# Kernel tuning notes

Hardware: AMD Instinct MI355X
Metric: run time of the kernel (lower is better)

The kernel has to match this reference:

```python
import jax, jax.numpy as jnp
import numpy as np

B, H, N, D, RPE = 2, 8, 4096, 64, 64
LAYERS = 3


def _rms(x):
    # SimpleRMSNorm: x / sqrt(mean(x^2) + eps), no learned scale
    return x / jnp.sqrt(jnp.mean(x * x, axis=-1, keepdims=True) + 1e-8)


def setup_inputs() -> dict:
    key = jax.random.key(0)
    ks = jax.random.split(key, 7)
    s = 1.0 / np.sqrt(RPE)
    return {
        "x": jax.random.normal(ks[0], (B, H, N, D), dtype=jnp.float32),
        "w_in": jax.random.normal(ks[1], (1, RPE), dtype=jnp.float32) * 0.5,
        "b_in": jax.random.normal(ks[2], (RPE,), dtype=jnp.float32) * 0.02,
        "w_hid": jax.random.normal(ks[3], (LAYERS, RPE, RPE), dtype=jnp.float32) * s,
        "b_hid": jax.random.normal(ks[4], (LAYERS, RPE), dtype=jnp.float32) * 0.02,
        "w_out": jax.random.normal(ks[5], (RPE, H * D), dtype=jnp.float32) * s,
        "b_out": jax.random.normal(ks[6], (H * D,), dtype=jnp.float32) * 0.02,
    }


def reference(x, w_in, b_in, w_hid, b_hid, w_out, b_out):
    n = x.shape[-2]
    dt = x.dtype

    def rpe(idx):  # idx: (m, 1) relative-position features
        h = idx @ w_in + b_in  # (m, RPE)
        for i in range(LAYERS):  # non-residual: x = layer(x)
            h = jax.nn.relu(_rms(h)) @ w_hid[i] + b_hid[i]
        h = jax.nn.relu(_rms(h)) @ w_out + b_out  # (m, H*D)
        return h.reshape(-1, H, D).transpose(1, 0, 2)  # (H, m, D)

    zero_idx = jnp.ones((1, 1), dt)
    pos_idx = (1.0 / jnp.arange(2, n + 1, dtype=dt)).reshape(n - 1, 1)
    neg_idx = (-1.0 / jnp.arange(n, 1, -1, dtype=dt)).reshape(n - 1, 1)

    zero_k = rpe(zero_idx)  # (H, 1, D); used for both T[0] slots like the torch code
    a = jnp.concatenate([zero_k, rpe(pos_idx), zero_k, rpe(neg_idx)], axis=1)  # (H, 2n, D)
    # act_type='none' -> identity activation on a

    # Toeplitz matvec as circular conv of length 2n via FFT
    y = jnp.fft.rfft(x, 2 * n, axis=-2)          # (B, H, n+1, D) complex
    v = jnp.fft.rfft(a, 2 * n, axis=-2)[None]    # (1, H, n+1, D) complex
    out = jnp.fft.irfft(v * y, 2 * n, axis=-2)[:, :, :n, :]
    return out.astype(dt)
```

## Files before the change

kernel.cpp:

```cpp
#include <hip/hip_runtime.h>

#define N_SEQ 4096
#define N_FFT 8192
#define LAYERS 3
#define FT 512
#define PIDX(i) ((i) + ((i) >> 5))

template<int M>
__device__ inline void pass16_fwd(float* re, float* im, int tid)
{
    const int Q = M >> 4;
    const int j = tid & (Q - 1);
    const int G = tid / Q;
    const int base = G * M + j;
    const float KR[4] = {1.f, 0.9238795325f, 0.7071067812f, 0.3826834324f};
    const float KI[4] = {0.f, -0.3826834324f, -0.7071067812f, -0.9238795325f};
    float xr[4][4], xi[4][4];
#pragma unroll
    for (int a = 0; a < 4; ++a)
#pragma unroll
        for (int b = 0; b < 4; ++b) {
            int idx = PIDX(base + a * (M >> 2) + b * Q);
            xr[a][b] = re[idx]; xi[a][b] = im[idx];
        }
    float cj, sj;
    __sincosf(-6.283185307179586f / (float)M * (float)j, &sj, &cj);
#pragma unroll
    for (int b = 0; b < 4; ++b) {
        float c1 = cj * KR[b] - sj * KI[b];
        float s1 = cj * KI[b] + sj * KR[b];
        float c2 = c1 * c1 - s1 * s1, s2 = 2.f * c1 * s1;
        float c3 = c2 * c1 - s2 * s1, s3 = c2 * s1 + s2 * c1;
        float ar = xr[0][b] + xr[2][b], ai = xi[0][b] + xi[2][b];
        float br = xr[0][b] - xr[2][b], bi = xi[0][b] - xi[2][b];
        float cr = xr[1][b] + xr[3][b], ci = xi[1][b] + xi[3][b];
        float dr = xi[1][b] - xi[3][b], di = -(xr[1][b] - xr[3][b]);
        xr[0][b] = ar + cr;               xi[0][b] = ai + ci;
        float t1r = br + dr, t1i = bi + di;
        xr[1][b] = t1r * c1 - t1i * s1;   xi[1][b] = t1r * s1 + t1i * c1;
        float t2r = ar - cr, t2i = ai - ci;
        xr[2][b] = t2r * c2 - t2i * s2;   xi[2][b] = t2r * s2 + t2i * c2;
        float t3r = br - dr, t3i = bi - di;
        xr[3][b] = t3r * c3 - t3i * s3;   xi[3][b] = t3r * s3 + t3i * c3;
    }
    {
        float e1c = cj * cj - sj * sj, e1s = 2.f * cj * sj;
        float c1 = e1c * e1c - e1s * e1s, s1 = 2.f * e1c * e1s;
        float c2 = c1 * c1 - s1 * s1, s2 = 2.f * c1 * s1;
        float c3 = c2 * c1 - s2 * s1, s3 = c2 * s1 + s2 * c1;
#pragma unroll
        for (int a = 0; a < 4; ++a) {
            float ar = xr[a][0] + xr[a][2], ai = xi[a][0] + xi[a][2];
            float br = xr[a][0] - xr[a][2], bi = xi[a][0] - xi[a][2];
            float cr = xr[a][1] + xr[a][3], ci = xi[a][1] + xi[a][3];
            float dr = xi[a][1] - xi[a][3], di = -(xr[a][1] - xr[a][3]);
            xr[a][0] = ar + cr;               xi[a][0] = ai + ci;
            float t1r = br + dr, t1i = bi + di;
            xr[a][1] = t1r * c1 - t1i * s1;   xi[a][1] = t1r * s1 + t1i * c1;
            float t2r = ar - cr, t2i = ai - ci;
            xr[a][2] = t2r * c2 - t2i * s2;   xi[a][2] = t2r * s2 + t2i * c2;
            float t3r = br - dr, t3i = bi - di;
            xr[a][3] = t3r * c3 - t3i * s3;   xi[a][3] = t3r * s3 + t3i * c3;
        }
    }
#pragma unroll
    for (int a = 0; a < 4; ++a)
#pragma unroll
        for (int b = 0; b < 4; ++b) {
            int idx = PIDX(base + a * (M >> 2) + b * Q);
            re[idx] = xr[a][b]; im[idx] = xi[a][b];
        }
}

template<int M>
__device__ inline void pass16_inv(float* re, float* im, int tid)
{
    const int Q = M >> 4;
    const int j = tid & (Q - 1);
    const int G = tid / Q;
    const int base = G * M + j;
    const float KR[4] = {1.f, 0.9238795325f, 0.7071067812f, 0.3826834324f};
    const float KI[4] = {0.f, 0.3826834324f, 0.7071067812f, 0.9238795325f};
    float xr[4][4], xi[4][4];
#pragma unroll
    for (int a = 0; a < 4; ++a)
#pragma unroll
        for (int b = 0; b < 4; ++b) {
            int idx = PIDX(base + a * (M >> 2) + b * Q);
            xr[a][b] = re[idx]; xi[a][b] = im[idx];
        }
    float cj, sj;
    __sincosf(6.283185307179586f / (float)M * (float)j, &sj, &cj);
    {
        float e1c = cj * cj - sj * sj, e1s = 2.f * cj * sj;
        float c1 = e1c * e1c - e1s * e1s, s1 = 2.f * e1c * e1s;
        float c2 = c1 * c1 - s1 * s1, s2 = 2.f * c1 * s1;
        float c3 = c2 * c1 - s2 * s1, s3 = c2 * s1 + s2 * c1;
#pragma unroll
        for (int a = 0; a < 4; ++a) {
            float t0r = xr[a][0], t0i = xi[a][0];
            float t1r = xr[a][1] * c1 - xi[a][1] * s1, t1i = xr[a][1] * s1 + xi[a][1] * c1;
            float t2r = xr[a][2] * c2 - xi[a][2] * s2, t2i = xr[a][2] * s2 + xi[a][2] * c2;
            float t3r = xr[a][3] * c3 - xi[a][3] * s3, t3i = xr[a][3] * s3 + xi[a][3] * c3;
            float pr = t0r + t2r, pi = t0i + t2i;
            float qr = t0r - t2r, qi = t0i - t2i;
            float rr = t1r + t3r, ri = t1i + t3i;
            float sr = -(t1i - t3i), si = t1r - t3r;
            xr[a][0] = pr + rr; xi[a][0] = pi + ri;
            xr[a][1] = qr + sr; xi[a][1] = qi + si;
            xr[a][2] = pr - rr; xi[a][2] = pi - ri;
            xr[a][3] = qr - sr; xi[a][3] = qi - si;
        }
    }
#pragma unroll
    for (int b = 0; b < 4; ++b) {
        float c1 = cj * KR[b] - sj * KI[b];
        float s1 = cj * KI[b] + sj * KR[b];
        float c2 = c1 * c1 - s1 * s1, s2 = 2.f * c1 * s1;
        float c3 = c2 * c1 - s2 * s1, s3 = c2 * s1 + s2 * c1;
        float t0r = xr[0][b], t0i = xi[0][b];
        float t1r = xr[1][b] * c1 - xi[1][b] * s1, t1i = xr[1][b] * s1 + xi[1][b] * c1;
        float t2r = xr[2][b] * c2 - xi[2][b] * s2, t2i = xr[2][b] * s2 + xi[2][b] * c2;
        float t3r = xr[3][b] * c3 - xi[3][b] * s3, t3i = xr[3][b] * s3 + xi[3][b] * c3;
        float pr = t0r + t2r, pi = t0i + t2i;
        float qr = t0r - t2r, qi = t0i - t2i;
        float rr = t1r + t3r, ri = t1i + t3i;
        float sr = -(t1i - t3i), si = t1r - t3r;
        xr[0][b] = pr + rr; xi[0][b] = pi + ri;
        xr[1][b] = qr + sr; xi[1][b] = qi + si;
        xr[2][b] = pr - rr; xi[2][b] = pi - ri;
        xr[3][b] = qr - sr; xi[3][b] = qi - si;
    }
#pragma unroll
    for (int a = 0; a < 4; ++a)
#pragma unroll
        for (int b = 0; b < 4; ++b) {
            int idx = PIDX(base + a * (M >> 2) + b * Q);
            re[idx] = xr[a][b]; im[idx] = xi[a][b];
        }
}

__device__ inline void fwd8(float* zr, float* zi, int o)
{
    const float R = 0.70710678118654752f;
    {
        float ar = zr[o] + zr[o+4], ai = zi[o] + zi[o+4];
        float br = zr[o] - zr[o+4], bi = zi[o] - zi[o+4];
        float cr = zr[o+2] + zr[o+6], ci = zi[o+2] + zi[o+6];
        float dr = zi[o+2] - zi[o+6], di = -(zr[o+2] - zr[o+6]);
        zr[o]   = ar + cr; zi[o]   = ai + ci;
        zr[o+2] = br + dr; zi[o+2] = bi + di;
        zr[o+4] = ar - cr; zi[o+4] = ai - ci;
        zr[o+6] = br - dr; zi[o+6] = bi - di;
    }
    {
        float ar = zr[o+1] + zr[o+5], ai = zi[o+1] + zi[o+5];
        float br = zr[o+1] - zr[o+5], bi = zi[o+1] - zi[o+5];
        float cr = zr[o+3] + zr[o+7], ci = zi[o+3] + zi[o+7];
        float dr = zi[o+3] - zi[o+7], di = -(zr[o+3] - zr[o+7]);
        zr[o+1] = ar + cr; zi[o+1] = ai + ci;
        float t1r = br + dr, t1i = bi + di;
        zr[o+3] = R * (t1r + t1i); zi[o+3] = R * (t1i - t1r);
        float t2r = ar - cr, t2i = ai - ci;
        zr[o+5] = t2i;  zi[o+5] = -t2r;
        float t3r = br - dr, t3i = bi - di;
        zr[o+7] = R * (t3i - t3r); zi[o+7] = -R * (t3r + t3i);
    }
#pragma unroll
    for (int p = 0; p < 8; p += 2) {
        float ur = zr[o+p], ui = zi[o+p], vr = zr[o+p+1], vi = zi[o+p+1];
        zr[o+p]   = ur + vr; zi[o+p]   = ui + vi;
        zr[o+p+1] = ur - vr; zi[o+p+1] = ui - vi;
    }
}

__device__ inline void inv8(float* zr, float* zi, int o)
{
    const float R = 0.70710678118654752f;
#pragma unroll
    for (int p = 0; p < 8; p += 2) {
        float ur = zr[o+p], ui = zi[o+p], vr = zr[o+p+1], vi = zi[o+p+1];
        zr[o+p]   = ur + vr; zi[o+p]   = ui + vi;
        zr[o+p+1] = ur - vr; zi[o+p+1] = ui - vi;
    }
    {
        float t0r = zr[o],   t0i = zi[o];
        float t1r = zr[o+2], t1i = zi[o+2];
        float t2r = zr[o+4], t2i = zi[o+4];
        float t3r = zr[o+6], t3i = zi[o+6];
        float pr = t0r + t2r, pi = t0i + t2i;
        float qr = t0r - t2r, qi = t0i - t2i;
        float rr = t1r + t3r, ri = t1i + t3i;
        float sr = -(t1i - t3i), si = t1r - t3r;
        zr[o]   = pr + rr; zi[o]   = pi + ri;
        zr[o+2] = qr + sr; zi[o+2] = qi + si;
        zr[o+4] = pr - rr; zi[o+4] = pi - ri;
        zr[o+6] = qr - sr; zi[o+6] = qi - si;
    }
    {
        float t0r = zr[o+1], t0i = zi[o+1];
        float yr = zr[o+3], yi = zi[o+3];
        float t1r = R * (yr - yi), t1i = R * (yr + yi);
        yr = zr[o+5]; yi = zi[o+5];
        float t2r = -yi, t2i = yr;
        yr = zr[o+7]; yi = zi[o+7];
        float t3r = -R * (yr + yi), t3i = R * (yr - yi);
        float pr = t0r + t2r, pi = t0i + t2i;
        float qr = t0r - t2r, qi = t0i - t2i;
        float rr = t1r + t3r, ri = t1i + t3i;
        float sr = -(t1i - t3i), si = t1r - t3r;
        zr[o+1] = pr + rr; zi[o+1] = pi + ri;
        zr[o+3] = qr + sr; zi[o+3] = qi + si;
        zr[o+5] = pr - rr; zi[o+5] = pi - ri;
        zr[o+7] = qr - sr; zi[o+7] = qi - si;
    }
}

__global__ __launch_bounds__(512, 4) void prep_kernel(
    const float* __restrict__ x,
    const float* __restrict__ w_in, const float* __restrict__ b_in,
    const float* __restrict__ w_hid, const float* __restrict__ b_hid,
    const float* __restrict__ w_out, const float* __restrict__ b_out,
    float* __restrict__ a_t, float2* __restrict__ xt2)
{
    __shared__ __align__(16) char smem[33536];
    const int tid = threadIdx.x;

    if (blockIdx.x >= 128) {
        float (*t0)[65] = (float (*)[65])smem;
        float (*t1)[65] = (float (*)[65])(smem + 16640);
        int bb = blockIdx.x - 128;
        int h = bb >> 6;
        int nb = bb & 63;
        int lx = tid & 63;
        int ly = tid >> 6;
        const float* s0 = x + ((size_t)h * N_SEQ + nb * 64) * 64;
        const float* s1 = x + ((size_t)(8 + h) * N_SEQ + nb * 64) * 64;
        for (int r = ly; r < 64; r += 8) {
            t0[r][lx] = s0[r * 64 + lx];
            t1[r][lx] = s1[r * 64 + lx];
        }
        __syncthreads();
        for (int r = ly; r < 64; r += 8) {
            float2* dst = xt2 + (size_t)(h * 64 + r) * N_SEQ + nb * 64;
            dst[lx] = make_float2(t0[lx][r], t1[lx][r]);
        }
        return;
    }

    float (*ubuf)[65] = (float (*)[65])smem;
    float (*sums)[9]  = (float (*)[9])(smem + 16640);
    const int p = tid & 63;
    const int w = __builtin_amdgcn_readfirstlane(tid >> 6);
    const int pos = blockIdx.x * 64 + p;

    float v;
    if (pos == 0 || pos == N_SEQ) v = 1.0f;
    else if (pos < N_SEQ)         v = 1.0f / (float)(pos + 1);
    else                          v = -1.0f / (float)(2 * N_SEQ + 1 - pos);

    float h[8];
#pragma unroll
    for (int i = 0; i < 8; ++i) {
        int f = w * 8 + i;
        h[i] = v * w_in[f] + b_in[f];
    }
    for (int L = 0; L < LAYERS; ++L) {
        float s = 0.f;
#pragma unroll
        for (int i = 0; i < 8; ++i) s += h[i] * h[i];
        sums[p][w] = s;
        __syncthreads();
        float tot = 0.f;
#pragma unroll
        for (int g = 0; g < 8; ++g) tot += sums[p][g];
        float r = rsqrtf(tot * (1.f / 64.f) + 1e-8f);
#pragma unroll
        for (int i = 0; i < 8; ++i)
            ubuf[p][w * 8 + i] = fmaxf(h[i] * r, 0.f);
        __syncthreads();
        float acc[8];
        const float* bh = b_hid + L * 64 + w * 8;
#pragma unroll
        for (int i = 0; i < 8; ++i) acc[i] = bh[i];
        const float* wbase = w_hid + L * 4096 + w * 8;
        for (int j = 0; j < 64; ++j) {
            float uj = ubuf[p][j];
            const float* wr = wbase + j * 64;
#pragma unroll
            for (int i = 0; i < 8; ++i)
                acc[i] = fmaf(uj, wr[i], acc[i]);
        }
#pragma unroll
        for (int i = 0; i < 8; ++i) h[i] = acc[i];
    }
    {
        float s = 0.f;
#pragma unroll
        for (int i = 0; i < 8; ++i) s += h[i] * h[i];
        sums[p][w] = s;
        __syncthreads();
        float tot = 0.f;
#pragma unroll
        for (int g = 0; g < 8; ++g) tot += sums[p][g];
        float r = rsqrtf(tot * (1.f / 64.f) + 1e-8f);
#pragma unroll
        for (int i = 0; i < 8; ++i)
            ubuf[p][w * 8 + i] = fmaxf(h[i] * r, 0.f);
        __syncthreads();
    }
    {
        const int c = w;
        float acc[64];
        const float* bo = b_out + c * 64;
#pragma unroll
        for (int f = 0; f < 64; ++f) acc[f] = bo[f];
        const float* wbase = w_out + c * 64;
        for (int j = 0; j < 64; ++j) {
            float uj = ubuf[p][j];
            const float* wr = wbase + j * 512;
#pragma unroll
            for (int f = 0; f < 64; ++f)
                acc[f] = fmaf(uj, wr[f], acc[f]);
        }
        float* dst = a_t + pos;
#pragma unroll
        for (int f = 0; f < 64; ++f)
            dst[(size_t)(c * 64 + f) * N_FFT] = acc[f];
    }
}

__global__ __launch_bounds__(FT, 2) void conv_kernel(const float* __restrict__ a_t,
                                                     const float2* __restrict__ xt2,
                                                     float2* __restrict__ out_t2)
{
    __shared__ float re[8448];
    __shared__ float im[8448];
    const int tid = threadIdx.x;
    const int hd = blockIdx.x;
    const float JR = 0.9238795325f;
    const float JI = -0.3826834324f;

    {
        const float* src = a_t + (size_t)hd * N_FFT;
        float ck, sk;
        __sincosf(-6.283185307179586f / 8192.f * (float)tid, &sk, &ck);
#pragma unroll
        for (int pp = 0; pp < 4; ++pp) {
            int k = pp * FT + tid;
            float x0 = src[k], x1 = src[k + 2048], x2 = src[k + 4096], x3 = src[k + 6144];
            float ar = x0 + x2, br = x0 - x2;
            float cr = x1 + x3, e = x1 - x3;
            re[PIDX(k)] = ar + cr; im[PIDX(k)] = 0.f;
            float c1 = ck, s1 = sk;
            float c2 = c1 * c1 - s1 * s1, s2 = 2.f * c1 * s1;
            float c3 = c2 * c1 - s2 * s1, s3 = c2 * s1 + s2 * c1;
            re[PIDX(k + 2048)] = br * c1 + e * s1;  im[PIDX(k + 2048)] = br * s1 - e * c1;
            float t2r = ar - cr;
            re[PIDX(k + 4096)] = t2r * c2;          im[PIDX(k + 4096)] = t2r * s2;
            re[PIDX(k + 6144)] = br * c3 - e * s3;  im[PIDX(k + 6144)] = br * s3 + e * c3;
            float tc = ck * JR - sk * JI; sk = ck * JI + sk * JR; ck = tc;
        }
    }
    __syncthreads();
    pass16_fwd<2048>(re, im, tid);
    __syncthreads();
    pass16_fwd<128>(re, im, tid);
    __syncthreads();
    float afr[16], afi[16];
    {
        const int base = tid * 16;
#pragma unroll
        for (int c = 0; c < 16; ++c) { int idx = PIDX(base + c); afr[c] = re[idx]; afi[c] = im[idx]; }
        fwd8(afr, afi, 0); fwd8(afr, afi, 8);
    }
    __syncthreads();
    {
        const float2* src = xt2 + (size_t)hd * N_SEQ;
        float ck, sk;
        __sincosf(-6.283185307179586f / 8192.f * (float)tid, &sk, &ck);
#pragma unroll
        for (int pp = 0; pp < 4; ++pp) {
            int k = pp * FT + tid;
            float2 z0 = src[k], z1 = src[k + 2048];
            float ar = z0.x, ai = z0.y;
            float cr = z1.x, ci = z1.y;
            float dr = z1.y, di = -z1.x;
            re[PIDX(k)] = ar + cr; im[PIDX(k)] = ai + ci;
            float c1 = ck, s1 = sk;
            float c2 = c1 * c1 - s1 * s1, s2 = 2.f * c1 * s1;
            float c3 = c2 * c1 - s2 * s1, s3 = c2 * s1 + s2 * c1;
            float t1r = ar + dr, t1i = ai + di;
            re[PIDX(k + 2048)] = t1r * c1 - t1i * s1; im[PIDX(k + 2048)] = t1r * s1 + t1i * c1;
            float t2r = ar - cr, t2i = ai - ci;
            re[PIDX(k + 4096)] = t2r * c2 - t2i * s2; im[PIDX(k + 4096)] = t2r * s2 + t2i * c2;
            float t3r = ar - dr, t3i = ai - di;
            re[PIDX(k + 6144)] = t3r * c3 - t3i * s3; im[PIDX(k + 6144)] = t3r * s3 + t3i * c3;
            float tc = ck * JR - sk * JI; sk = ck * JI + sk * JR; ck = tc;
        }
    }
    __syncthreads();
    pass16_fwd<2048>(re, im, tid);
    __syncthreads();
    pass16_fwd<128>(re, im, tid);
    __syncthreads();
    {
        const int base = tid * 16;
        float zr[16], zi[16];
#pragma unroll
        for (int c = 0; c < 16; ++c) { int idx = PIDX(base + c); zr[c] = re[idx]; zi[c] = im[idx]; }
        fwd8(zr, zi, 0); fwd8(zr, zi, 8);
        const float inv = 1.0f / (float)N_FFT;
#pragma unroll
        for (int c = 0; c < 16; ++c) {
            float xr = zr[c], xi_ = zi[c];
            zr[c] = (xr * afr[c] - xi_ * afi[c]) * inv;
            zi[c] = (xr * afi[c] + xi_ * afr[c]) * inv;
        }
        inv8(zr, zi, 0); inv8(zr, zi, 8);
#pragma unroll
        for (int c = 0; c < 16; ++c) { int idx = PIDX(base + c); re[idx] = zr[c]; im[idx] = zi[c]; }
    }
    __syncthreads();
    pass16_inv<128>(re, im, tid);
    __syncthreads();
    pass16_inv<2048>(re, im, tid);
    __syncthreads();
    {
        float2* dst = out_t2 + (size_t)hd * N_SEQ;
        float ck, sk;
        __sincosf(6.283185307179586f / 8192.f * (float)tid, &sk, &ck);
        const float JcR = 0.9238795325f, JcI = 0.3826834324f;
#pragma unroll
        for (int pp = 0; pp < 4; ++pp) {
            int k = pp * FT + tid;
            float c1 = ck, s1 = sk;
            float c2 = c1 * c1 - s1 * s1, s2 = 2.f * c1 * s1;
            float c3 = c2 * c1 - s2 * s1, s3 = c2 * s1 + s2 * c1;
            float t0r = re[PIDX(k)],        t0i = im[PIDX(k)];
            float y1r = re[PIDX(k + 2048)], y1i = im[PIDX(k + 2048)];
            float y2r = re[PIDX(k + 4096)], y2i = im[PIDX(k + 4096)];
            float y3r = re[PIDX(k + 6144)], y3i = im[PIDX(k + 6144)];
            float t1r = y1r * c1 - y1i * s1, t1i = y1r * s1 + y1i * c1;
            float t2r = y2r * c2 - y2i * s2, t2i = y2r * s2 + y2i * c2;
            float t3r = y3r * c3 - y3i * s3, t3i = y3r * s3 + y3i * c3;
            float pr = t0r + t2r, pi = t0i + t2i;
            float qr = t0r - t2r, qi = t0i - t2i;
            float rr = t1r + t3r, ri = t1i + t3i;
            float sr = -(t1i - t3i), si = t1r - t3r;
            dst[k]        = make_float2(pr + rr, pi + ri);
            dst[k + 2048] = make_float2(qr + sr, qi + si);
            float tc = ck * JcR - sk * JcI; sk = ck * JcI + sk * JcR; ck = tc;
        }
    }
}

__global__ __launch_bounds__(256) void transpose_o_kernel(const float2* __restrict__ out_t2,
                                                          float* __restrict__ out)
{
    __shared__ float t0[64][65];
    __shared__ float t1[64][65];
    int h = blockIdx.x >> 6;
    int nb = blockIdx.x & 63;
    int lx = threadIdx.x & 63;
    int ly = threadIdx.x >> 6;
    for (int r = ly; r < 64; r += 4) {
        float2 v = out_t2[(size_t)(h * 64 + r) * N_SEQ + nb * 64 + lx];
        t0[r][lx] = v.x;
        t1[r][lx] = v.y;
    }
    __syncthreads();
    float* d0 = out + ((size_t)h * N_SEQ + nb * 64) * 64;
    float* d1 = out + ((size_t)(8 + h) * N_SEQ + nb * 64) * 64;
    for (int r = ly; r < 64; r += 4) {
        d0[r * 64 + lx] = t0[lx][r];
        d1[r * 64 + lx] = t1[lx][r];
    }
}

extern "C" void kernel_launch(void* const* d_in, const int* in_sizes, int n_in,
                              void* d_out, int out_size, void* d_ws, size_t ws_size,
                              hipStream_t stream)
{
    const float* x     = (const float*)d_in[0];
    const float* w_in  = (const float*)d_in[1];
    const float* b_in  = (const float*)d_in[2];
    const float* w_hid = (const float*)d_in[3];
    const float* b_hid = (const float*)d_in[4];
    const float* w_out = (const float*)d_in[5];
    const float* b_out = (const float*)d_in[6];
    float* out = (float*)d_out;

    char* ws = (char*)d_ws;
    float2* xt2    = (float2*)ws;
    float*  a_t    = (float*)(ws + (size_t)16 * 1024 * 1024);
    float2* out_t2 = (float2*)(ws + (size_t)32 * 1024 * 1024);

    prep_kernel<<<640, 512, 0, stream>>>(x, w_in, b_in, w_hid, b_hid, w_out, b_out,
                                         a_t, xt2);
    conv_kernel<<<512, FT, 0, stream>>>(a_t, xt2, out_t2);
    transpose_o_kernel<<<512, 256, 0, stream>>>(out_t2, out);
}
```

Measured before the change: 160.6 us.

## Register-tile prep MLP matmuls and halve prep block size

Result: slower. 164.2 us (+2.2%).

```diff
diff --git a/kernel.cpp b/kernel.cpp
--- a/kernel.cpp
+++ b/kernel.cpp
@@ -216,7 +216,7 @@
     }
 }
 
-__global__ __launch_bounds__(512, 4) void prep_kernel(
+__global__ __launch_bounds__(256, 2) void prep_kernel(
     const float* __restrict__ x,
     const float* __restrict__ w_in, const float* __restrict__ b_in,
     const float* __restrict__ w_hid, const float* __restrict__ b_hid,
@@ -236,97 +236,134 @@
         int ly = tid >> 6;
         const float* s0 = x + ((size_t)h * N_SEQ + nb * 64) * 64;
         const float* s1 = x + ((size_t)(8 + h) * N_SEQ + nb * 64) * 64;
-        for (int r = ly; r < 64; r += 8) {
+        for (int r = ly; r < 64; r += 4) {
             t0[r][lx] = s0[r * 64 + lx];
             t1[r][lx] = s1[r * 64 + lx];
         }
         __syncthreads();
-        for (int r = ly; r < 64; r += 8) {
+        for (int r = ly; r < 64; r += 4) {
             float2* dst = xt2 + (size_t)(h * 64 + r) * N_SEQ + nb * 64;
             dst[lx] = make_float2(t0[lx][r], t1[lx][r]);
         }
         return;
     }
 
-    float (*ubuf)[65] = (float (*)[65])smem;
-    float (*sums)[9]  = (float (*)[9])(smem + 16640);
-    const int p = tid & 63;
-    const int w = __builtin_amdgcn_readfirstlane(tid >> 6);
-    const int pos = blockIdx.x * 64 + p;
-
-    float v;
-    if (pos == 0 || pos == N_SEQ) v = 1.0f;
-    else if (pos < N_SEQ)         v = 1.0f / (float)(pos + 1);
-    else                          v = -1.0f / (float)(2 * N_SEQ + 1 - pos);
-
-    float h[8];
-#pragma unroll
-    for (int i = 0; i < 8; ++i) {
-        int f = w * 8 + i;
-        h[i] = v * w_in[f] + b_in[f];
-    }
-    for (int L = 0; L < LAYERS; ++L) {
-        float s = 0.f;
-#pragma unroll
-        for (int i = 0; i < 8; ++i) s += h[i] * h[i];
-        sums[p][w] = s;
-        __syncthreads();
-        float tot = 0.f;
-#pragma unroll
-        for (int g = 0; g < 8; ++g) tot += sums[p][g];
-        float r = rsqrtf(tot * (1.f / 64.f) + 1e-8f);
-#pragma unroll
-        for (int i = 0; i < 8; ++i)
-            ubuf[p][w * 8 + i] = fmaxf(h[i] * r, 0.f);
-        __syncthreads();
-        float acc[8];
-        const float* bh = b_hid + L * 64 + w * 8;
-#pragma unroll
-        for (int i = 0; i < 8; ++i) acc[i] = bh[i];
-        const float* wbase = w_hid + L * 4096 + w * 8;
-        for (int j = 0; j < 64; ++j) {
-            float uj = ubuf[p][j];
-            const float* wr = wbase + j * 64;
-#pragma unroll
-            for (int i = 0; i < 8; ++i)
-                acc[i] = fmaf(uj, wr[i], acc[i]);
-        }
-#pragma unroll
-        for (int i = 0; i < 8; ++i) h[i] = acc[i];
-    }
-    {
-        float s = 0.f;
-#pragma unroll
-        for (int i = 0; i < 8; ++i) s += h[i] * h[i];
-        sums[p][w] = s;
-        __syncthreads();
-        float tot = 0.f;
-#pragma unroll
-        for (int g = 0; g < 8; ++g) tot += sums[p][g];
-        float r = rsqrtf(tot * (1.f / 64.f) + 1e-8f);
-#pragma unroll
-        for (int i = 0; i < 8; ++i)
-            ubuf[p][w * 8 + i] = fmaxf(h[i] * r, 0.f);
-        __syncthreads();
-    }
-    {
-        const int c = w;
-        float acc[64];
-        const float* bo = b_out + c * 64;
-#pragma unroll
-        for (int f = 0; f < 64; ++f) acc[f] = bo[f];
-        const float* wbase = w_out + c * 64;
-        for (int j = 0; j < 64; ++j) {
-            float uj = ubuf[p][j];
-            const float* wr = wbase + j * 512;
-#pragma unroll
-            for (int f = 0; f < 64; ++f)
-                acc[f] = fmaf(uj, wr[f], acc[f]);
-        }
-        float* dst = a_t + pos;
-#pragma unroll
-        for (int f = 0; f < 64; ++f)
-            dst[(size_t)(c * 64 + f) * N_FFT] = acc[f];
+    float (*ubuf)[68] = (float (*)[68])smem;
+    float (*sums)[68] = (float (*)[68])(smem + 17408);
+    const int pos0 = blockIdx.x * 64;
+
+    {
+        const int pq = tid & 15;
+        const int fq = tid >> 4;
+        float v[4];
+#pragma unroll
+        for (int k = 0; k < 4; ++k) {
+            int pos = pos0 + pq * 4 + k;
+            if (pos == 0 || pos == N_SEQ) v[k] = 1.0f;
+            else if (pos < N_SEQ)         v[k] = 1.0f / (float)(pos + 1);
+            else                          v[k] = -1.0f / (float)(2 * N_SEQ + 1 - pos);
+        }
+        float h[4][4];
+#pragma unroll
+        for (int i = 0; i < 4; ++i) {
+            float wi = w_in[fq * 4 + i], bi = b_in[fq * 4 + i];
+#pragma unroll
+            for (int k = 0; k < 4; ++k) h[i][k] = v[k] * wi + bi;
+        }
+        for (int L = 0; L <= LAYERS; ++L) {
+            float4 ss = make_float4(0.f, 0.f, 0.f, 0.f);
+#pragma unroll
+            for (int i = 0; i < 4; ++i) {
+                ss.x += h[i][0] * h[i][0]; ss.y += h[i][1] * h[i][1];
+                ss.z += h[i][2] * h[i][2]; ss.w += h[i][3] * h[i][3];
+            }
+            *(float4*)&sums[fq][pq * 4] = ss;
+            __syncthreads();
+            float4 tot = make_float4(0.f, 0.f, 0.f, 0.f);
+#pragma unroll
+            for (int g = 0; g < 16; ++g) {
+                float4 s4 = *(const float4*)&sums[g][pq * 4];
+                tot.x += s4.x; tot.y += s4.y; tot.z += s4.z; tot.w += s4.w;
+            }
+            float r[4] = {rsqrtf(tot.x * (1.f/64.f) + 1e-8f),
+                          rsqrtf(tot.y * (1.f/64.f) + 1e-8f),
+                          rsqrtf(tot.z * (1.f/64.f) + 1e-8f),
+                          rsqrtf(tot.w * (1.f/64.f) + 1e-8f)};
+#pragma unroll
+            for (int i = 0; i < 4; ++i) {
+                float4 u4;
+                u4.x = fmaxf(h[i][0] * r[0], 0.f);
+                u4.y = fmaxf(h[i][1] * r[1], 0.f);
+                u4.z = fmaxf(h[i][2] * r[2], 0.f);
+                u4.w = fmaxf(h[i][3] * r[3], 0.f);
+                *(float4*)&ubuf[fq * 4 + i][pq * 4] = u4;
+            }
+            __syncthreads();
+            if (L == LAYERS) break;
+            float acc[4][4];
+#pragma unroll
+            for (int i = 0; i < 4; ++i) {
+                float bi = b_hid[L * 64 + fq * 4 + i];
+#pragma unroll
+                for (int k = 0; k < 4; ++k) acc[i][k] = bi;
+            }
+            const float* wb = w_hid + L * 4096 + fq * 4;
+#pragma unroll 4
+            for (int j = 0; j < 64; ++j) {
+                float4 u4 = *(const float4*)&ubuf[j][pq * 4];
+                float4 w4 = *(const float4*)(wb + j * 64);
+                acc[0][0] = fmaf(u4.x, w4.x, acc[0][0]); acc[0][1] = fmaf(u4.y, w4.x, acc[0][1]);
+                acc[0][2] = fmaf(u4.z, w4.x, acc[0][2]); acc[0][3] = fmaf(u4.w, w4.x, acc[0][3]);
+                acc[1][0] = fmaf(u4.x, w4.y, acc[1][0]); acc[1][1] = fmaf(u4.y, w4.y, acc[1][1]);
+                acc[1][2] = fmaf(u4.z, w4.y, acc[1][2]); acc[1][3] = fmaf(u4.w, w4.y, acc[1][3]);
+                acc[2][0] = fmaf(u4.x, w4.z, acc[2][0]); acc[2][1] = fmaf(u4.y, w4.z, acc[2][1]);
+                acc[2][2] = fmaf(u4.z, w4.z, acc[2][2]); acc[2][3] = fmaf(u4.w, w4.z, acc[2][3]);
+                acc[3][0] = fmaf(u4.x, w4.w, acc[3][0]); acc[3][1] = fmaf(u4.y, w4.w, acc[3][1]);
+                acc[3][2] = fmaf(u4.z, w4.w, acc[3][2]); acc[3][3] = fmaf(u4.w, w4.w, acc[3][3]);
+            }
+#pragma unroll
+            for (int i = 0; i < 4; ++i)
+#pragma unroll
+                for (int k = 0; k < 4; ++k) h[i][k] = acc[i][k];
+        }
+    }
+
+    {
+        const int wv = tid >> 6;
+        const int lane = tid & 63;
+        const int po = lane & 7;
+        const int fo = lane >> 3;
+        for (int rnd = 0; rnd < 2; ++rnd) {
+            const int c = rnd * 4 + wv;
+            float acc[8][8];
+#pragma unroll
+            for (int i = 0; i < 8; ++i) {
+                float bo = b_out[c * 64 + fo * 8 + i];
+#pragma unroll
+                for (int k = 0; k < 8; ++k) acc[i][k] = bo;
+            }
+            const float* wb = w_out + c * 64 + fo * 8;
+#pragma unroll 2
+            for (int j = 0; j < 64; ++j) {
+                float4 u0 = *(const float4*)&ubuf[j][po * 8];
+                float4 u1 = *(const float4*)&ubuf[j][po * 8 + 4];
+                float4 w0 = *(const float4*)(wb + j * 512);
+                float4 w1 = *(const float4*)(wb + j * 512 + 4);
+                float wv_[8] = {w0.x, w0.y, w0.z, w0.w, w1.x, w1.y, w1.z, w1.w};
+                float uv_[8] = {u0.x, u0.y, u0.z, u0.w, u1.x, u1.y, u1.z, u1.w};
+#pragma unroll
+                for (int i = 0; i < 8; ++i)
+#pragma unroll
+                    for (int k = 0; k < 8; ++k)
+                        acc[i][k] = fmaf(uv_[k], wv_[i], acc[i][k]);
+            }
+#pragma unroll
+            for (int i = 0; i < 8; ++i) {
+                float* dst = a_t + (size_t)(c * 64 + fo * 8 + i) * N_FFT + pos0 + po * 8;
+                *(float4*)dst       = make_float4(acc[i][0], acc[i][1], acc[i][2], acc[i][3]);
+                *(float4*)(dst + 4) = make_float4(acc[i][4], acc[i][5], acc[i][6], acc[i][7]);
+            }
+        }
     }
 }
 
@@ -496,7 +533,7 @@
     float*  a_t    = (float*)(ws + (size_t)16 * 1024 * 1024);
     float2* out_t2 = (float2*)(ws + (size_t)32 * 1024 * 1024);
 
-    prep_kernel<<<640, 512, 0, stream>>>(x, w_in, b_in, w_hid, b_hid, w_out, b_out,
+    prep_kernel<<<640, 256, 0, stream>>>(x, w_in, b_in, w_hid, b_hid, w_out, b_out,
                                          a_t, xt2);
     conv_kernel<<<512, FT, 0, stream>>>(a_t, xt2, out_t2);
     transpose_o_kernel<<<512, 256, 0, stream>>>(out_t2, out);
```

## Retile RPE MLP prep kernel with register-blocked output GEMM and vector stores

Applied to the files above, without the earlier changes.

New measurement: 159.5 us. About the same (-0.7%).

```diff
diff --git a/kernel.cpp b/kernel.cpp
--- a/kernel.cpp
+++ b/kernel.cpp
@@ -216,7 +216,7 @@
     }
 }
 
-__global__ __launch_bounds__(512, 4) void prep_kernel(
+__global__ __launch_bounds__(256, 2) void prep_kernel(
     const float* __restrict__ x,
     const float* __restrict__ w_in, const float* __restrict__ b_in,
     const float* __restrict__ w_hid, const float* __restrict__ b_hid,
@@ -226,107 +226,112 @@
     __shared__ __align__(16) char smem[33536];
     const int tid = threadIdx.x;
 
-    if (blockIdx.x >= 128) {
+    if (blockIdx.x >= 256) {
         float (*t0)[65] = (float (*)[65])smem;
         float (*t1)[65] = (float (*)[65])(smem + 16640);
-        int bb = blockIdx.x - 128;
+        int bb = blockIdx.x - 256;
         int h = bb >> 6;
         int nb = bb & 63;
         int lx = tid & 63;
         int ly = tid >> 6;
         const float* s0 = x + ((size_t)h * N_SEQ + nb * 64) * 64;
         const float* s1 = x + ((size_t)(8 + h) * N_SEQ + nb * 64) * 64;
-        for (int r = ly; r < 64; r += 8) {
+        for (int r = ly; r < 64; r += 4) {
             t0[r][lx] = s0[r * 64 + lx];
             t1[r][lx] = s1[r * 64 + lx];
         }
         __syncthreads();
-        for (int r = ly; r < 64; r += 8) {
+        for (int r = ly; r < 64; r += 4) {
             float2* dst = xt2 + (size_t)(h * 64 + r) * N_SEQ + nb * 64;
             dst[lx] = make_float2(t0[lx][r], t1[lx][r]);
         }
         return;
     }
 
-    float (*ubuf)[65] = (float (*)[65])smem;
-    float (*sums)[9]  = (float (*)[9])(smem + 16640);
-    const int p = tid & 63;
-    const int w = __builtin_amdgcn_readfirstlane(tid >> 6);
-    const int pos = blockIdx.x * 64 + p;
-
-    float v;
-    if (pos == 0 || pos == N_SEQ) v = 1.0f;
-    else if (pos < N_SEQ)         v = 1.0f / (float)(pos + 1);
-    else                          v = -1.0f / (float)(2 * N_SEQ + 1 - pos);
-
-    float h[8];
-#pragma unroll
-    for (int i = 0; i < 8; ++i) {
-        int f = w * 8 + i;
-        h[i] = v * w_in[f] + b_in[f];
-    }
-    for (int L = 0; L < LAYERS; ++L) {
-        float s = 0.f;
-#pragma unroll
-        for (int i = 0; i < 8; ++i) s += h[i] * h[i];
-        sums[p][w] = s;
-        __syncthreads();
-        float tot = 0.f;
-#pragma unroll
-        for (int g = 0; g < 8; ++g) tot += sums[p][g];
-        float r = rsqrtf(tot * (1.f / 64.f) + 1e-8f);
-#pragma unroll
-        for (int i = 0; i < 8; ++i)
-            ubuf[p][w * 8 + i] = fmaxf(h[i] * r, 0.f);
-        __syncthreads();
-        float acc[8];
-        const float* bh = b_hid + L * 64 + w * 8;
-#pragma unroll
-        for (int i = 0; i < 8; ++i) acc[i] = bh[i];
-        const float* wbase = w_hid + L * 4096 + w * 8;
-        for (int j = 0; j < 64; ++j) {
-            float uj = ubuf[p][j];
-            const float* wr = wbase + j * 64;
+    float (*ubuf)[36] = (float (*)[36])smem;
+    float (*sums)[9]  = (float (*)[9])(smem + 9216);
+    const int pos0 = blockIdx.x * 32;
+
+    {
+        const int p  = tid & 31;
+        const int fp = tid >> 5;
+        const int pos = pos0 + p;
+        float v;
+        if (pos == 0 || pos == N_SEQ) v = 1.0f;
+        else if (pos < N_SEQ)         v = 1.0f / (float)(pos + 1);
+        else                          v = -1.0f / (float)(2 * N_SEQ + 1 - pos);
+
+        float h[8];
+#pragma unroll
+        for (int i = 0; i < 8; ++i) {
+            int f = fp * 8 + i;
+            h[i] = v * w_in[f] + b_in[f];
+        }
+        for (int L = 0; L <= LAYERS; ++L) {
+            float s = 0.f;
+#pragma unroll
+            for (int i = 0; i < 8; ++i) s += h[i] * h[i];
+            sums[p][fp] = s;
+            __syncthreads();
+            float tot = 0.f;
+#pragma unroll
+            for (int g = 0; g < 8; ++g) tot += sums[p][g];
+            float r = rsqrtf(tot * (1.f / 64.f) + 1e-8f);
 #pragma unroll
             for (int i = 0; i < 8; ++i)
-                acc[i] = fmaf(uj, wr[i], acc[i]);
-        }
-#pragma unroll
-        for (int i = 0; i < 8; ++i) h[i] = acc[i];
-    }
-    {
-        float s = 0.f;
-#pragma unroll
-        for (int i = 0; i < 8; ++i) s += h[i] * h[i];
-        sums[p][w] = s;
-        __syncthreads();
-        float tot = 0.f;
-#pragma unroll
-        for (int g = 0; g < 8; ++g) tot += sums[p][g];
-        float r = rsqrtf(tot * (1.f / 64.f) + 1e-8f);
-#pragma unroll
-        for (int i = 0; i < 8; ++i)
-            ubuf[p][w * 8 + i] = fmaxf(h[i] * r, 0.f);
-        __syncthreads();
-    }
-    {
-        const int c = w;
-        float acc[64];
-        const float* bo = b_out + c * 64;
-#pragma unroll
-        for (int f = 0; f < 64; ++f) acc[f] = bo[f];
-        const float* wbase = w_out + c * 64;
-        for (int j = 0; j < 64; ++j) {
-            float uj = ubuf[p][j];
-            const float* wr = wbase + j * 512;
-#pragma unroll
-            for (int f = 0; f < 64; ++f)
-                acc[f] = fmaf(uj, wr[f], acc[f]);
-        }
-        float* dst = a_t + pos;
-#pragma unroll
-        for (int f = 0; f < 64; ++f)
-            dst[(size_t)(c * 64 + f) * N_FFT] = acc[f];
+                ubuf[fp * 8 + i][p] = fmaxf(h[i] * r, 0.f);
+            __syncthreads();
+            if (L == LAYERS) break;
+            float acc[8];
+#pragma unroll
+            for (int i = 0; i < 8; ++i) acc[i] = b_hid[L * 64 + fp * 8 + i];
+            const float* wb = w_hid + L * 4096 + fp * 8;
+#pragma unroll 4
+            for (int j = 0; j < 64; ++j) {
+                float uj = ubuf[j][p];
+                float4 w0 = *(const float4*)(wb + j * 64);
+                float4 w1 = *(const float4*)(wb + j * 64 + 4);
+                acc[0] = fmaf(uj, w0.x, acc[0]); acc[1] = fmaf(uj, w0.y, acc[1]);
+                acc[2] = fmaf(uj, w0.z, acc[2]); acc[3] = fmaf(uj, w0.w, acc[3]);
+                acc[4] = fmaf(uj, w1.x, acc[4]); acc[5] = fmaf(uj, w1.y, acc[5]);
+                acc[6] = fmaf(uj, w1.z, acc[6]); acc[7] = fmaf(uj, w1.w, acc[7]);
+            }
+#pragma unroll
+            for (int i = 0; i < 8; ++i) h[i] = acc[i];
+        }
+    }
+
+    {
+        const int p4 = tid & 7;
+        const int of = tid >> 3;
+        for (int co = 0; co < 4; ++co) {
+            float acc[4][4];
+#pragma unroll
+            for (int i = 0; i < 4; ++i) {
+                float bo = b_out[co * 128 + of * 4 + i];
+#pragma unroll
+                for (int k = 0; k < 4; ++k) acc[i][k] = bo;
+            }
+            const float* wb = w_out + co * 128 + of * 4;
+#pragma unroll 4
+            for (int j = 0; j < 64; ++j) {
+                float4 u4 = *(const float4*)&ubuf[j][p4 * 4];
+                float4 w4 = *(const float4*)(wb + j * 512);
+                acc[0][0] = fmaf(u4.x, w4.x, acc[0][0]); acc[0][1] = fmaf(u4.y, w4.x, acc[0][1]);
+                acc[0][2] = fmaf(u4.z, w4.x, acc[0][2]); acc[0][3] = fmaf(u4.w, w4.x, acc[0][3]);
+                acc[1][0] = fmaf(u4.x, w4.y, acc[1][0]); acc[1][1] = fmaf(u4.y, w4.y, acc[1][1]);
+                acc[1][2] = fmaf(u4.z, w4.y, acc[1][2]); acc[1][3] = fmaf(u4.w, w4.y, acc[1][3]);
+                acc[2][0] = fmaf(u4.x, w4.z, acc[2][0]); acc[2][1] = fmaf(u4.y, w4.z, acc[2][1]);
+                acc[2][2] = fmaf(u4.z, w4.z, acc[2][2]); acc[2][3] = fmaf(u4.w, w4.z, acc[2][3]);
+                acc[3][0] = fmaf(u4.x, w4.w, acc[3][0]); acc[3][1] = fmaf(u4.y, w4.w, acc[3][1]);
+                acc[3][2] = fmaf(u4.z, w4.w, acc[3][2]); acc[3][3] = fmaf(u4.w, w4.w, acc[3][3]);
+            }
+#pragma unroll
+            for (int i = 0; i < 4; ++i) {
+                float* dst = a_t + (size_t)(co * 128 + of * 4 + i) * N_FFT + pos0 + p4 * 4;
+                *(float4*)dst = make_float4(acc[i][0], acc[i][1], acc[i][2], acc[i][3]);
+            }
+        }
     }
 }
 
@@ -496,7 +501,7 @@
     float*  a_t    = (float*)(ws + (size_t)16 * 1024 * 1024);
     float2* out_t2 = (float2*)(ws + (size_t)32 * 1024 * 1024);
 
-    prep_kernel<<<640, 512, 0, stream>>>(x, w_in, b_in, w_hid, b_hid, w_out, b_out,
+    prep_kernel<<<768, 256, 0, stream>>>(x, w_in, b_in, w_hid, b_hid, w_out, b_out,
                                          a_t, xt2);
     conv_kernel<<<512, FT, 0, stream>>>(a_t, xt2, out_t2);
     transpose_o_kernel<<<512, 256, 0, stream>>>(out_t2, out);
```
